# Kernel tuning notes

Hardware: AMD Instinct MI355X
Metric: run time of the kernel (lower is better)

## Reference

```python
import jax, jax.numpy as jnp
import numpy as np

DIM = 1024
HEADS = 16
DIM_HEAD = 64
INNER = HEADS * DIM_HEAD
SCALE = DIM_HEAD ** -0.5


def rotate_half(t):
    # '... (j d) -> ... j d' with j=2: split last dim in half
    x1, x2 = jnp.split(t, 2, axis=-1)
    return jnp.concatenate((-x2, x1), axis=-1)


def rotary_pos(n, d, dtype):
    inv_freq = 1.0 / (10000.0 ** (jnp.arange(0, d, 2, dtype=jnp.float32) / d))
    freqs = jnp.arange(n, dtype=jnp.float32)[:, None] * inv_freq[None, :]  # (n, d/2)
    return jnp.concatenate((freqs, freqs), axis=-1).astype(dtype)  # (n, d)


def apply_rope(pos, t):
    return t * jnp.cos(pos) + rotate_half(t) * jnp.sin(pos)


def setup_inputs() -> dict:
    key = jax.random.key(0)
    ks = jax.random.split(key, 5)
    x = jax.random.normal(ks[0], (2, 2048, DIM), dtype=jnp.float32)
    gamma = jnp.ones((DIM,), dtype=jnp.float32)
    beta = jnp.zeros((DIM,), dtype=jnp.float32)
    Wq = jax.random.normal(ks[1], (DIM, INNER), dtype=jnp.float32) * 0.02
    Wkv = jax.random.normal(ks[2], (DIM, 2 * INNER), dtype=jnp.float32) * 0.02
    Wo = jax.random.normal(ks[3], (INNER, DIM), dtype=jnp.float32) * 0.02
    return {"x": x, "gamma": gamma, "beta": beta, "Wq": Wq, "Wkv": Wkv, "Wo": Wo}


def reference(x, gamma, beta, Wq, Wkv, Wo):
    b, n, _ = x.shape
    # LayerNorm with learned gamma, fixed-zero beta buffer
    mu = jnp.mean(x, axis=-1, keepdims=True)
    var = jnp.var(x, axis=-1, keepdims=True)
    xn = (x - mu) / jnp.sqrt(var + 1e-5) * gamma + beta

    q = xn @ Wq                       # (b, n, inner)
    kv = xn @ Wkv
    k, v = jnp.split(kv, 2, axis=-1)

    def to_heads(t):
        return t.reshape(b, n, HEADS, DIM_HEAD).transpose(0, 2, 1, 3)  # b h n d

    q, k, v = map(to_heads, (q, k, v))

    pos = rotary_pos(n, DIM_HEAD, x.dtype)  # (n, d)
    q = apply_rope(pos, q)
    k = apply_rope(pos, k)

    q = q * SCALE
    sim = jnp.einsum('bhid,bhjd->bhij', q, k)

    neg = -jnp.finfo(sim.dtype).max
    causal_mask = jnp.triu(jnp.ones((n, n), dtype=bool), k=1)
    sim = jnp.where(causal_mask, neg, sim)

    attn = jax.nn.softmax(sim, axis=-1)
    out = jnp.einsum('bhij,bhjd->bhid', attn, v)
    out = out.transpose(0, 2, 1, 3).reshape(b, n, INNER)
    return out @ Wo
```

## Files before the change

### kernel.cpp

```cpp
#include <hip/hip_runtime.h>
#include <stdint.h>

typedef unsigned short u16;
typedef __attribute__((ext_vector_type(8))) short short8;
typedef __attribute__((ext_vector_type(4))) float floatx4;
typedef __attribute__((ext_vector_type(4))) unsigned short u16x4;
typedef __attribute__((ext_vector_type(2))) unsigned int uint2v;

__device__ __forceinline__ float bf2f(u16 v) {
  union { uint32_t u; float f; } x; x.u = ((uint32_t)v) << 16; return x.f;
}
__device__ __forceinline__ u16 f2bf(float f) {
  union { float f; uint32_t u; } x; x.f = f;
  uint32_t r = x.u + 0x7fffu + ((x.u >> 16) & 1u);
  return (u16)(r >> 16);
}
__device__ __forceinline__ uint32_t fu(float f) {
  union { float f; uint32_t u; } x; x.f = f; return x.u;
}

#define GL2LDS(g, l)                                                          \
  __builtin_amdgcn_global_load_lds(                                           \
      (const __attribute__((address_space(1))) void*)(g),                     \
      (__attribute__((address_space(3))) void*)(l), 16, 0, 0)

__global__ __launch_bounds__(256) void transpose_w3_k(const float* __restrict__ Wq,
                                                      const float* __restrict__ Wkv,
                                                      const float* __restrict__ Wo,
                                                      u16* __restrict__ wqkvT,
                                                      u16* __restrict__ woT) {
  __shared__ float tile[32][33];
  int z = blockIdx.z;
  const float* in = (z == 0) ? Wq : (z == 1) ? Wkv : Wo;
  u16* out = (z == 0) ? wqkvT : (z == 1) ? (wqkvT + 1024 * 1024) : woT;
  int C = (z == 1) ? 2048 : 1024;
  int c0 = blockIdx.x * 32, r0 = blockIdx.y * 32;
  if (c0 >= C) return;
  int tx = threadIdx.x, ty = threadIdx.y;
#pragma unroll
  for (int i = 0; i < 32; i += 8)
    tile[ty + i][tx] = in[(size_t)(r0 + ty + i) * C + c0 + tx];
  __syncthreads();
#pragma unroll
  for (int i = 0; i < 32; i += 8)
    out[(size_t)(c0 + ty + i) * 1024 + r0 + tx] = f2bf(tile[tx][ty + i]);
}

__global__ __launch_bounds__(256) void layernorm_k(const float* __restrict__ x,
                                                   const float* __restrict__ gamma,
                                                   const float* __restrict__ beta,
                                                   u16* __restrict__ xn) {
  int row = blockIdx.x;
  int t = threadIdx.x;
  const float* xr = x + (size_t)row * 1024;
  float4 xv = *(const float4*)(xr + t * 4);
  float v0 = xv.x, v1 = xv.y, v2 = xv.z, v3 = xv.w;
  float s = v0 + v1 + v2 + v3;
  float s2 = v0 * v0 + v1 * v1 + v2 * v2 + v3 * v3;
#pragma unroll
  for (int d = 1; d < 64; d <<= 1) {
    s += __shfl_xor(s, d, 64);
    s2 += __shfl_xor(s2, d, 64);
  }
  __shared__ float red[8];
  int lane = t & 63, wv = t >> 6;
  if (lane == 0) { red[wv] = s; red[4 + wv] = s2; }
  __syncthreads();
  s = red[0] + red[1] + red[2] + red[3];
  s2 = red[4] + red[5] + red[6] + red[7];
  float mu = s * (1.0f / 1024.0f);
  float var = s2 * (1.0f / 1024.0f) - mu * mu;
  float rstd = rsqrtf(var + 1e-5f);
  float4 gv = *(const float4*)(gamma + t * 4);
  float4 bv = *(const float4*)(beta + t * 4);
  u16x4 ov;
  ov.x = f2bf((v0 - mu) * rstd * gv.x + bv.x);
  ov.y = f2bf((v1 - mu) * rstd * gv.y + bv.y);
  ov.z = f2bf((v2 - mu) * rstd * gv.z + bv.z);
  ov.w = f2bf((v3 - mu) * rstd * gv.w + bv.w);
  *(u16x4*)(xn + (size_t)row * 1024 + t * 4) = ov;
}

__global__ __launch_bounds__(256) void gemm_bf16_k(const u16* __restrict__ A,
                                                   const u16* __restrict__ BT,
                                                   void* __restrict__ Cp,
                                                   int K, int lda, int ldc,
                                                   int f32out) {
  __shared__ __align__(16) u16 lA[128 * 32];
  __shared__ __align__(16) u16 lB[128 * 32];
  int tid = threadIdx.x;
  int bm = blockIdx.y * 128;
  int bn = blockIdx.x * 128;
  int w = tid >> 6, l = tid & 63;
  int wm = (w >> 1) * 64, wn = (w & 1) * 64;
  int lr = l & 15, lq = l >> 4;
  floatx4 acc[4][4] = {};
  int sr = w * 16 + (l >> 2);
  int sc = (l & 3) * 8;
  for (int k0 = 0; k0 < K; k0 += 32) {
    GL2LDS(A + (size_t)(bm + sr) * lda + k0 + sc, &lA[sr * 32 + sc]);
    GL2LDS(A + (size_t)(bm + sr + 64) * lda + k0 + sc, &lA[(sr + 64) * 32 + sc]);
    GL2LDS(BT + (size_t)(bn + sr) * K + k0 + sc, &lB[sr * 32 + sc]);
    GL2LDS(BT + (size_t)(bn + sr + 64) * K + k0 + sc, &lB[(sr + 64) * 32 + sc]);
    __syncthreads();
    short8 afr[4], bfr[4];
#pragma unroll
    for (int i = 0; i < 4; i++)
      afr[i] = *(const short8*)(&lA[(wm + i * 16 + lr) * 32 + lq * 8]);
#pragma unroll
    for (int i = 0; i < 4; i++)
      bfr[i] = *(const short8*)(&lB[(wn + i * 16 + lr) * 32 + lq * 8]);
#pragma unroll
    for (int mi = 0; mi < 4; mi++)
#pragma unroll
      for (int ni = 0; ni < 4; ni++)
        acc[mi][ni] = __builtin_amdgcn_mfma_f32_16x16x32_bf16(
            afr[mi], bfr[ni], acc[mi][ni], 0, 0, 0);
    __syncthreads();
  }
  if (f32out) {
    float* Cf = (float*)Cp;
#pragma unroll
    for (int mi = 0; mi < 4; mi++)
#pragma unroll
      for (int ni = 0; ni < 4; ni++)
#pragma unroll
        for (int r = 0; r < 4; r++) {
          int row = bm + wm + mi * 16 + lq * 4 + r;
          int col = bn + wn + ni * 16 + lr;
          Cf[(size_t)row * ldc + col] = acc[mi][ni][r];
        }
  } else {
    u16* Cb = (u16*)Cp;
#pragma unroll
    for (int mi = 0; mi < 4; mi++)
#pragma unroll
      for (int ni = 0; ni < 4; ni++)
#pragma unroll
        for (int r = 0; r < 4; r++) {
          int row = bm + wm + mi * 16 + lq * 4 + r;
          int col = bn + wn + ni * 16 + lr;
          Cb[(size_t)row * ldc + col] = f2bf(acc[mi][ni][r]);
        }
  }
}

__global__ __launch_bounds__(256) void gemm64_bf16_k(const u16* __restrict__ A,
                                                     const u16* __restrict__ BT,
                                                     float* __restrict__ C,
                                                     int K, int lda, int ldc) {
  __shared__ __align__(16) u16 lA[64 * 32];
  __shared__ __align__(16) u16 lB[128 * 32];
  int tid = threadIdx.x;
  int bm = blockIdx.y * 64;
  int bn = blockIdx.x * 128;
  int w = tid >> 6, l = tid & 63;
  int wm = (w >> 1) * 32, wn = (w & 1) * 64;
  int lr = l & 15, lq = l >> 4;
  floatx4 acc[2][4] = {};
  int sr = w * 16 + (l >> 2);
  int sc = (l & 3) * 8;
  for (int k0 = 0; k0 < K; k0 += 32) {
    GL2LDS(A + (size_t)(bm + sr) * lda + k0 + sc, &lA[sr * 32 + sc]);
    GL2LDS(BT + (size_t)(bn + sr) * K + k0 + sc, &lB[sr * 32 + sc]);
    GL2LDS(BT + (size_t)(bn + sr + 64) * K + k0 + sc, &lB[(sr + 64) * 32 + sc]);
    __syncthreads();
    short8 afr[2], bfr[4];
#pragma unroll
    for (int i = 0; i < 2; i++)
      afr[i] = *(const short8*)(&lA[(wm + i * 16 + lr) * 32 + lq * 8]);
#pragma unroll
    for (int i = 0; i < 4; i++)
      bfr[i] = *(const short8*)(&lB[(wn + i * 16 + lr) * 32 + lq * 8]);
#pragma unroll
    for (int mi = 0; mi < 2; mi++)
#pragma unroll
      for (int ni = 0; ni < 4; ni++)
        acc[mi][ni] = __builtin_amdgcn_mfma_f32_16x16x32_bf16(
            afr[mi], bfr[ni], acc[mi][ni], 0, 0, 0);
    __syncthreads();
  }
#pragma unroll
  for (int mi = 0; mi < 2; mi++)
#pragma unroll
    for (int ni = 0; ni < 4; ni++)
#pragma unroll
      for (int r = 0; r < 4; r++) {
        int row = bm + wm + mi * 16 + lq * 4 + r;
        int col = bn + wn + ni * 16 + lr;
        C[(size_t)row * ldc + col] = acc[mi][ni][r];
      }
}

__global__ __launch_bounds__(256) void rope_inplace_k(u16* __restrict__ qkv) {
  int idx = blockIdx.x * 256 + threadIdx.x;
  int ig = idx & 7;
  int h = (idx >> 3) & 15;
  int row = idx >> 7;
  int n = row & 2047;
  int i0 = ig * 4;
  const float QS = 0.125f * 1.44269504088896f;
  float c_[4], s_[4];
  float invf = exp2f(-(float)i0 * 0.4152410118609203f);
  const float rstep = 0.74989420933245582f;
#pragma unroll
  for (int e = 0; e < 4; e++) {
    float ang = (float)n * invf;
    c_[e] = cosf(ang);
    s_[e] = sinf(ang);
    invf *= rstep;
  }
  size_t base = (size_t)row * 3072 + h * 64 + i0;
  u16x4 qlo = *(u16x4*)(qkv + base);
  u16x4 qhi = *(u16x4*)(qkv + base + 32);
  u16x4 klo = *(u16x4*)(qkv + base + 1024);
  u16x4 khi = *(u16x4*)(qkv + base + 1056);
  u16x4 oqlo, oqhi, oklo, okhi;
#pragma unroll
  for (int e = 0; e < 4; e++) {
    float x1 = bf2f(((u16*)&qlo)[e]), x2 = bf2f(((u16*)&qhi)[e]);
    ((u16*)&oqlo)[e] = f2bf((x1 * c_[e] - x2 * s_[e]) * QS);
    ((u16*)&oqhi)[e] = f2bf((x2 * c_[e] + x1 * s_[e]) * QS);
    x1 = bf2f(((u16*)&klo)[e]); x2 = bf2f(((u16*)&khi)[e]);
    ((u16*)&oklo)[e] = f2bf(x1 * c_[e] - x2 * s_[e]);
    ((u16*)&okhi)[e] = f2bf(x2 * c_[e] + x1 * s_[e]);
  }
  *(u16x4*)(qkv + base) = oqlo;
  *(u16x4*)(qkv + base + 32) = oqhi;
  *(u16x4*)(qkv + base + 1024) = oklo;
  *(u16x4*)(qkv + base + 1056) = okhi;
}

__global__ __launch_bounds__(256) void transpose_v_k(const u16* __restrict__ qkv,
                                                     u16* __restrict__ vT) {
  __shared__ u16 tile[32][33];
  int bh = blockIdx.z;
  int b = bh >> 4, h = bh & 15;
  int n0 = blockIdx.x * 32, d0 = blockIdx.y * 32;
  int tx = threadIdx.x, ty = threadIdx.y;
#pragma unroll
  for (int i = 0; i < 32; i += 8)
    tile[ty + i][tx] =
        qkv[(size_t)(b * 2048 + n0 + ty + i) * 3072 + 2048 + h * 64 + d0 + tx];
  __syncthreads();
#pragma unroll
  for (int i = 0; i < 32; i += 8)
    vT[((size_t)bh * 64 + d0 + ty + i) * 2048 + n0 + tx] = tile[tx][ty + i];
}

#define LPT 72
__device__ __forceinline__ void attn_tile2(const u16* lK, const u16* lV, u16* lp,
                                           const short8* aq, floatx4* o,
                                           float& m_i, float& l_i, int lr, int lq,
                                           bool diag, int q0, int k0g,
                                           short8 ones) {
  floatx4 s[4];
#pragma unroll
  for (int ni = 0; ni < 4; ni++) {
    floatx4 a = {};
#pragma unroll
    for (int kc = 0; kc < 2; kc++) {
      int R = ni * 16 + lr;
      int c8 = (kc * 4 + lq) ^ (R & 7);
      short8 kf = *(const short8*)&lK[R * 64 + c8 * 8];
      a = __builtin_amdgcn_mfma_f32_16x16x32_bf16(kf, aq[kc], a, 0, 0, 0);
    }
    s[ni] = a;
  }
  if (diag) {
    int qg = q0 + lr;
#pragma unroll
    for (int ni = 0; ni < 4; ni++)
#pragma unroll
      for (int r = 0; r < 4; r++) {
        int kg = k0g + ni * 16 + lq * 4 + r;
        if (kg > qg) s[ni][r] = -1e30f;
      }
  }
  float mx = fmaxf(fmaxf(s[0][0], s[0][1]), fmaxf(s[0][2], s[0][3]));
#pragma unroll
  for (int ni = 1; ni < 4; ni++)
    mx = fmaxf(mx, fmaxf(fmaxf(s[ni][0], s[ni][1]), fmaxf(s[ni][2], s[ni][3])));
  mx = fmaxf(mx, __shfl_xor(mx, 16, 64));
  mx = fmaxf(mx, __shfl_xor(mx, 32, 64));
  float mnew = fmaxf(m_i, mx);
  float alpha = exp2f(m_i - mnew);
  m_i = mnew;
#pragma unroll
  for (int ni = 0; ni < 4; ni++) {
    float p0 = exp2f(s[ni][0] - mnew), p1 = exp2f(s[ni][1] - mnew);
    float p2 = exp2f(s[ni][2] - mnew), p3 = exp2f(s[ni][3] - mnew);
    uint2v dw;
    dw.x = __builtin_amdgcn_perm(fu(p1), fu(p0), 0x07060302u);
    dw.y = __builtin_amdgcn_perm(fu(p3), fu(p2), 0x07060302u);
    *(uint2v*)&lp[lr * LPT + ni * 16 + lq * 4] = dw;
  }
  short8 pb0 = *(const short8*)&lp[lr * LPT + lq * 8];
  short8 pb1 = *(const short8*)&lp[lr * LPT + 32 + lq * 8];
  floatx4 z = {};
  z = __builtin_amdgcn_mfma_f32_16x16x32_bf16(ones, pb0, z, 0, 0, 0);
  z = __builtin_amdgcn_mfma_f32_16x16x32_bf16(ones, pb1, z, 0, 0, 0);
  l_i = l_i * alpha + z[0];
#pragma unroll
  for (int di = 0; di < 4; di++)
#pragma unroll
    for (int r = 0; r < 4; r++) o[di][r] *= alpha;
#pragma unroll
  for (int di = 0; di < 4; di++) {
    int R = di * 16 + lr;
    int c80 = lq ^ (R & 7);
    int c81 = (4 + lq) ^ (R & 7);
    short8 v0 = *(const short8*)&lV[R * 64 + c80 * 8];
    o[di] = __builtin_amdgcn_mfma_f32_16x16x32_bf16(v0, pb0, o[di], 0, 0, 0);
    short8 v1 = *(const short8*)&lV[R * 64 + c81 * 8];
    o[di] = __builtin_amdgcn_mfma_f32_16x16x32_bf16(v1, pb1, o[di], 0, 0, 0);
  }
}

__global__ __launch_bounds__(256) void attn_k(const u16* __restrict__ qkv,
                                              const u16* __restrict__ vt,
                                              u16* __restrict__ out) {
  __shared__ __align__(16) u16 lK[2][64 * 64];
  __shared__ __align__(16) u16 lV[2][64 * 64];
  __shared__ __align__(16) u16 lP[4][16 * LPT];
  int bh = blockIdx.y;
  int b = bh >> 4, h = bh & 15;
  int p = blockIdx.x;
  int jB = 31 - p;
  int tid = threadIdx.x;
  int w = tid >> 6, l = tid & 63;
  int lr = l & 15, lq = l >> 4;
  int q0A = p * 64 + w * 16;
  int q0B = jB * 64 + w * 16;
  const u16* qb = qkv + (size_t)b * 2048 * 3072 + h * 64;
  const u16* kb = qkv + (size_t)b * 2048 * 3072 + 1024 + h * 64;
  const u16* vb = vt + (size_t)bh * 64 * 2048;
  short8 aqA[2], aqB[2];
  aqA[0] = *(const short8*)(qb + (size_t)(q0A + lr) * 3072 + lq * 8);
  aqA[1] = *(const short8*)(qb + (size_t)(q0A + lr) * 3072 + 32 + lq * 8);
  aqB[0] = *(const short8*)(qb + (size_t)(q0B + lr) * 3072 + lq * 8);
  aqB[1] = *(const short8*)(qb + (size_t)(q0B + lr) * 3072 + 32 + lq * 8);
  short8 ones;
#pragma unroll
  for (int i = 0; i < 8; i++) ones[i] = (short)0x3F80;
  floatx4 oA[4] = {}, oB[4] = {};
  float mA = -1e30f, lA_ = 0.0f, mB = -1e30f, lB_ = 0.0f;
  int srow8 = l >> 3;
  int sc8 = (l & 7) ^ srow8;
  u16* lp = &lP[w][0];
  auto stage = [&](int bufi, int kt) {
#pragma unroll
    for (int c = 0; c < 2; c++) {
      int m = w + c * 4;
      int row = m * 8 + srow8;
      GL2LDS(kb + (size_t)(kt * 64 + row) * 3072 + sc8 * 8, &lK[bufi][m * 512]);
      GL2LDS(vb + (size_t)row * 2048 + kt * 64 + sc8 * 8, &lV[bufi][m * 512]);
    }
  };
  stage(0, 0);
  for (int kt = 0; kt <= jB; ++kt) {
    int cur = kt & 1;
    __syncthreads();
    if (kt < jB) stage(cur ^ 1, kt + 1);
    attn_tile2(lK[cur], lV[cur], lp, aqB, oB, mB, lB_, lr, lq, kt == jB, q0B,
               kt * 64, ones);
    if (kt <= p)
      attn_tile2(lK[cur], lV[cur], lp, aqA, oA, mA, lA_, lr, lq, kt == p, q0A,
                 kt * 64, ones);
  }
  float rlA = 1.0f / lA_, rlB = 1.0f / lB_;
#pragma unroll
  for (int di = 0; di < 4; di++) {
    uint2v dwA, dwB;
    u16 a0 = f2bf(oA[di][0] * rlA), a1 = f2bf(oA[di][1] * rlA);
    u16 a2 = f2bf(oA[di][2] * rlA), a3 = f2bf(oA[di][3] * rlA);
    dwA.x = (uint32_t)a0 | ((uint32_t)a1 << 16);
    dwA.y = (uint32_t)a2 | ((uint32_t)a3 << 16);
    u16 b0 = f2bf(oB[di][0] * rlB), b1 = f2bf(oB[di][1] * rlB);
    u16 b2 = f2bf(oB[di][2] * rlB), b3 = f2bf(oB[di][3] * rlB);
    dwB.x = (uint32_t)b0 | ((uint32_t)b1 << 16);
    dwB.y = (uint32_t)b2 | ((uint32_t)b3 << 16);
    int dcol = h * 64 + di * 16 + lq * 4;
    *(uint2v*)(out + ((size_t)(b * 2048 + q0A + lr)) * 3072 + dcol) = dwA;
    *(uint2v*)(out + ((size_t)(b * 2048 + q0B + lr)) * 3072 + dcol) = dwB;
  }
}

extern "C" void kernel_launch(void* const* d_in, const int* in_sizes, int n_in,
                              void* d_out, int out_size, void* d_ws, size_t ws_size,
                              hipStream_t stream) {
  const float* x = (const float*)d_in[0];
  const float* gamma = (const float*)d_in[1];
  const float* beta = (const float*)d_in[2];
  const float* Wq = (const float*)d_in[3];
  const float* Wkv = (const float*)d_in[4];
  const float* Wo = (const float*)d_in[5];
  float* out = (float*)d_out;
  char* ws = (char*)d_ws;

  u16* qkv = (u16*)(ws);
  u16* wqkvT = (u16*)(ws + 25165824);
  u16* woT = (u16*)(ws + 31457280);
  u16* xn = (u16*)(ws + 33554432);
  u16* vT = xn;
  u16* attn_out = qkv + 2048;

  dim3 tb32(32, 8);
  transpose_w3_k<<<dim3(64, 32, 3), tb32, 0, stream>>>(Wq, Wkv, Wo, wqkvT, woT);
  layernorm_k<<<4096, 256, 0, stream>>>(x, gamma, beta, xn);
  gemm_bf16_k<<<dim3(24, 32), 256, 0, stream>>>(xn, wqkvT, qkv, 1024, 1024, 3072, 0);
  rope_inplace_k<<<2048, 256, 0, stream>>>(qkv);
  transpose_v_k<<<dim3(64, 2, 32), tb32, 0, stream>>>(qkv, vT);
  attn_k<<<dim3(16, 32), 256, 0, stream>>>(qkv, vT, attn_out);
  gemm64_bf16_k<<<dim3(8, 64), 256, 0, stream>>>(attn_out, woT, out, 1024, 3072, 1024);
}
```

Measured before the change: 214.3 us.

## Fuse RoPE and V-transpose kernels; hoist K/V fragments to registers in attention

Merges the in-place RoPE kernel and the V transpose kernel into one launch, splitting work by block index, which removes one kernel launch. In the attention loop, K and V fragments are read from LDS once per tile into registers and shared by both query halves instead of being reloaded for each. Separate per-wave P buffers for the A and B halves remove the reuse hazard between the two tile calls. Holding the fragments in registers raises register pressure and may lower occupancy.

Measured after the change: 215.9 us. About the same (+0.8%).

```diff
diff --git a/kernel.cpp b/kernel.cpp
--- a/kernel.cpp
+++ b/kernel.cpp
@@ -192,64 +192,70 @@
       }
 }
 
-__global__ __launch_bounds__(256) void rope_inplace_k(u16* __restrict__ qkv) {
-  int idx = blockIdx.x * 256 + threadIdx.x;
-  int ig = idx & 7;
-  int h = (idx >> 3) & 15;
-  int row = idx >> 7;
-  int n = row & 2047;
-  int i0 = ig * 4;
-  const float QS = 0.125f * 1.44269504088896f;
-  float c_[4], s_[4];
-  float invf = exp2f(-(float)i0 * 0.4152410118609203f);
-  const float rstep = 0.74989420933245582f;
-#pragma unroll
-  for (int e = 0; e < 4; e++) {
-    float ang = (float)n * invf;
-    c_[e] = cosf(ang);
-    s_[e] = sinf(ang);
-    invf *= rstep;
-  }
-  size_t base = (size_t)row * 3072 + h * 64 + i0;
-  u16x4 qlo = *(u16x4*)(qkv + base);
-  u16x4 qhi = *(u16x4*)(qkv + base + 32);
-  u16x4 klo = *(u16x4*)(qkv + base + 1024);
-  u16x4 khi = *(u16x4*)(qkv + base + 1056);
-  u16x4 oqlo, oqhi, oklo, okhi;
-#pragma unroll
-  for (int e = 0; e < 4; e++) {
-    float x1 = bf2f(((u16*)&qlo)[e]), x2 = bf2f(((u16*)&qhi)[e]);
-    ((u16*)&oqlo)[e] = f2bf((x1 * c_[e] - x2 * s_[e]) * QS);
-    ((u16*)&oqhi)[e] = f2bf((x2 * c_[e] + x1 * s_[e]) * QS);
-    x1 = bf2f(((u16*)&klo)[e]); x2 = bf2f(((u16*)&khi)[e]);
-    ((u16*)&oklo)[e] = f2bf(x1 * c_[e] - x2 * s_[e]);
-    ((u16*)&okhi)[e] = f2bf(x2 * c_[e] + x1 * s_[e]);
-  }
-  *(u16x4*)(qkv + base) = oqlo;
-  *(u16x4*)(qkv + base + 32) = oqhi;
-  *(u16x4*)(qkv + base + 1024) = oklo;
-  *(u16x4*)(qkv + base + 1056) = okhi;
-}
-
-__global__ __launch_bounds__(256) void transpose_v_k(const u16* __restrict__ qkv,
-                                                     u16* __restrict__ vT) {
-  __shared__ u16 tile[32][33];
-  int bh = blockIdx.z;
-  int b = bh >> 4, h = bh & 15;
-  int n0 = blockIdx.x * 32, d0 = blockIdx.y * 32;
-  int tx = threadIdx.x, ty = threadIdx.y;
-#pragma unroll
-  for (int i = 0; i < 32; i += 8)
-    tile[ty + i][tx] =
-        qkv[(size_t)(b * 2048 + n0 + ty + i) * 3072 + 2048 + h * 64 + d0 + tx];
-  __syncthreads();
-#pragma unroll
-  for (int i = 0; i < 32; i += 8)
-    vT[((size_t)bh * 64 + d0 + ty + i) * 2048 + n0 + tx] = tile[tx][ty + i];
+__global__ __launch_bounds__(256) void rope_vt_k(u16* __restrict__ qkv,
+                                                 u16* __restrict__ vT) {
+  int bid = blockIdx.x;
+  if (bid < 2048) {
+    int idx = bid * 256 + threadIdx.x;
+    int ig = idx & 7;
+    int h = (idx >> 3) & 15;
+    int row = idx >> 7;
+    int n = row & 2047;
+    int i0 = ig * 4;
+    const float QS = 0.125f * 1.44269504088896f;
+    float c_[4], s_[4];
+    float invf = exp2f(-(float)i0 * 0.4152410118609203f);
+    const float rstep = 0.74989420933245582f;
+#pragma unroll
+    for (int e = 0; e < 4; e++) {
+      float ang = (float)n * invf;
+      c_[e] = cosf(ang);
+      s_[e] = sinf(ang);
+      invf *= rstep;
+    }
+    size_t base = (size_t)row * 3072 + h * 64 + i0;
+    u16x4 qlo = *(u16x4*)(qkv + base);
+    u16x4 qhi = *(u16x4*)(qkv + base + 32);
+    u16x4 klo = *(u16x4*)(qkv + base + 1024);
+    u16x4 khi = *(u16x4*)(qkv + base + 1056);
+    u16x4 oqlo, oqhi, oklo, okhi;
+#pragma unroll
+    for (int e = 0; e < 4; e++) {
+      float x1 = bf2f(((u16*)&qlo)[e]), x2 = bf2f(((u16*)&qhi)[e]);
+      ((u16*)&oqlo)[e] = f2bf((x1 * c_[e] - x2 * s_[e]) * QS);
+      ((u16*)&oqhi)[e] = f2bf((x2 * c_[e] + x1 * s_[e]) * QS);
+      x1 = bf2f(((u16*)&klo)[e]); x2 = bf2f(((u16*)&khi)[e]);
+      ((u16*)&oklo)[e] = f2bf(x1 * c_[e] - x2 * s_[e]);
+      ((u16*)&okhi)[e] = f2bf(x2 * c_[e] + x1 * s_[e]);
+    }
+    *(u16x4*)(qkv + base) = oqlo;
+    *(u16x4*)(qkv + base + 32) = oqhi;
+    *(u16x4*)(qkv + base + 1024) = oklo;
+    *(u16x4*)(qkv + base + 1056) = okhi;
+  } else {
+    __shared__ u16 tile[32][33];
+    int vb = bid - 2048;
+    int bh = vb >> 7;
+    int rest = vb & 127;
+    int d0 = (rest >> 6) * 32;
+    int n0 = (rest & 63) * 32;
+    int b = bh >> 4, h = bh & 15;
+    int tid = threadIdx.x;
+    int tx = tid & 31, ty = tid >> 5;
+#pragma unroll
+    for (int i = 0; i < 32; i += 8)
+      tile[ty + i][tx] =
+          qkv[(size_t)(b * 2048 + n0 + ty + i) * 3072 + 2048 + h * 64 + d0 + tx];
+    __syncthreads();
+#pragma unroll
+    for (int i = 0; i < 32; i += 8)
+      vT[((size_t)bh * 64 + d0 + ty + i) * 2048 + n0 + tx] = tile[tx][ty + i];
+  }
 }
 
 #define LPT 72
-__device__ __forceinline__ void attn_tile2(const u16* lK, const u16* lV, u16* lp,
+__device__ __forceinline__ void attn_tile2(const short8 kf[4][2],
+                                           const short8 vf[4][2], u16* lp,
                                            const short8* aq, floatx4* o,
                                            float& m_i, float& l_i, int lr, int lq,
                                            bool diag, int q0, int k0g,
@@ -259,12 +265,8 @@
   for (int ni = 0; ni < 4; ni++) {
     floatx4 a = {};
 #pragma unroll
-    for (int kc = 0; kc < 2; kc++) {
-      int R = ni * 16 + lr;
-      int c8 = (kc * 4 + lq) ^ (R & 7);
-      short8 kf = *(const short8*)&lK[R * 64 + c8 * 8];
-      a = __builtin_amdgcn_mfma_f32_16x16x32_bf16(kf, aq[kc], a, 0, 0, 0);
-    }
+    for (int kc = 0; kc < 2; kc++)
+      a = __builtin_amdgcn_mfma_f32_16x16x32_bf16(kf[ni][kc], aq[kc], a, 0, 0, 0);
     s[ni] = a;
   }
   if (diag) {
@@ -307,13 +309,8 @@
     for (int r = 0; r < 4; r++) o[di][r] *= alpha;
 #pragma unroll
   for (int di = 0; di < 4; di++) {
-    int R = di * 16 + lr;
-    int c80 = lq ^ (R & 7);
-    int c81 = (4 + lq) ^ (R & 7);
-    short8 v0 = *(const short8*)&lV[R * 64 + c80 * 8];
-    o[di] = __builtin_amdgcn_mfma_f32_16x16x32_bf16(v0, pb0, o[di], 0, 0, 0);
-    short8 v1 = *(const short8*)&lV[R * 64 + c81 * 8];
-    o[di] = __builtin_amdgcn_mfma_f32_16x16x32_bf16(v1, pb1, o[di], 0, 0, 0);
+    o[di] = __builtin_amdgcn_mfma_f32_16x16x32_bf16(vf[di][0], pb0, o[di], 0, 0, 0);
+    o[di] = __builtin_amdgcn_mfma_f32_16x16x32_bf16(vf[di][1], pb1, o[di], 0, 0, 0);
   }
 }
 
@@ -322,7 +319,8 @@
                                               u16* __restrict__ out) {
   __shared__ __align__(16) u16 lK[2][64 * 64];
   __shared__ __align__(16) u16 lV[2][64 * 64];
-  __shared__ __align__(16) u16 lP[4][16 * LPT];
+  __shared__ __align__(16) u16 lPA[4][16 * LPT];
+  __shared__ __align__(16) u16 lPB[4][16 * LPT];
   int bh = blockIdx.y;
   int b = bh >> 4, h = bh & 15;
   int p = blockIdx.x;
@@ -347,7 +345,6 @@
   float mA = -1e30f, lA_ = 0.0f, mB = -1e30f, lB_ = 0.0f;
   int srow8 = l >> 3;
   int sc8 = (l & 7) ^ srow8;
-  u16* lp = &lP[w][0];
   auto stage = [&](int bufi, int kt) {
 #pragma unroll
     for (int c = 0; c < 2; c++) {
@@ -362,10 +359,21 @@
     int cur = kt & 1;
     __syncthreads();
     if (kt < jB) stage(cur ^ 1, kt + 1);
-    attn_tile2(lK[cur], lV[cur], lp, aqB, oB, mB, lB_, lr, lq, kt == jB, q0B,
+    short8 kf[4][2], vf[4][2];
+#pragma unroll
+    for (int ni = 0; ni < 4; ni++) {
+      int R = ni * 16 + lr;
+      int c80 = (lq ^ (R & 7)) * 8;
+      int c81 = ((4 + lq) ^ (R & 7)) * 8;
+      kf[ni][0] = *(const short8*)&lK[cur][R * 64 + c80];
+      kf[ni][1] = *(const short8*)&lK[cur][R * 64 + c81];
+      vf[ni][0] = *(const short8*)&lV[cur][R * 64 + c80];
+      vf[ni][1] = *(const short8*)&lV[cur][R * 64 + c81];
+    }
+    attn_tile2(kf, vf, &lPB[w][0], aqB, oB, mB, lB_, lr, lq, kt == jB, q0B,
                kt * 64, ones);
     if (kt <= p)
-      attn_tile2(lK[cur], lV[cur], lp, aqA, oA, mA, lA_, lr, lq, kt == p, q0A,
+      attn_tile2(kf, vf, &lPA[w][0], aqA, oA, mA, lA_, lr, lq, kt == p, q0A,
                  kt * 64, ones);
   }
   float rlA = 1.0f / lA_, rlB = 1.0f / lB_;
@@ -409,8 +417,7 @@
   transpose_w3_k<<<dim3(64, 32, 3), tb32, 0, stream>>>(Wq, Wkv, Wo, wqkvT, woT);
   layernorm_k<<<4096, 256, 0, stream>>>(x, gamma, beta, xn);
   gemm_bf16_k<<<dim3(24, 32), 256, 0, stream>>>(xn, wqkvT, qkv, 1024, 1024, 3072, 0);
-  rope_inplace_k<<<2048, 256, 0, stream>>>(qkv);
-  transpose_v_k<<<dim3(64, 2, 32), tb32, 0, stream>>>(qkv, vT);
+  rope_vt_k<<<6144, 256, 0, stream>>>(qkv, vT);
   attn_k<<<dim3(16, 32), 256, 0, stream>>>(qkv, vT, attn_out);
   gemm64_bf16_k<<<dim3(8, 64), 256, 0, stream>>>(attn_out, woT, out, 1024, 3072, 1024);
 }
```

## Fuse RoPE into QKV GEMM epilogue and merge layernorm with weight transpose

Applied to the files above, without the earlier changes.

RoPE rotation and the query scaling move into the QKV GEMM epilogue. Each wave's 64-column tile covers one head, so the x1/x2 halves are already in registers (acc[ni] and acc[ni+2]), which removes the separate in-place RoPE pass over qkv. Layernorm and the three weight transposes are merged into one launch by splitting on block index, and the V transpose uses a flattened 1D grid. The result is two fewer kernel launches and one less read-modify-write of Q/K. In exchange the epilogue uses fast __sincosf in fp32 on the unrounded accumulator, which may shift numerics slightly.

New measurement: 216.2 us. Within noise of the previous version (+0.9%).

```diff
diff --git a/kernel.cpp b/kernel.cpp
--- a/kernel.cpp
+++ b/kernel.cpp
@@ -24,68 +24,72 @@
       (const __attribute__((address_space(1))) void*)(g),                     \
       (__attribute__((address_space(3))) void*)(l), 16, 0, 0)
 
-__global__ __launch_bounds__(256) void transpose_w3_k(const float* __restrict__ Wq,
-                                                      const float* __restrict__ Wkv,
-                                                      const float* __restrict__ Wo,
-                                                      u16* __restrict__ wqkvT,
-                                                      u16* __restrict__ woT) {
-  __shared__ float tile[32][33];
-  int z = blockIdx.z;
-  const float* in = (z == 0) ? Wq : (z == 1) ? Wkv : Wo;
-  u16* out = (z == 0) ? wqkvT : (z == 1) ? (wqkvT + 1024 * 1024) : woT;
-  int C = (z == 1) ? 2048 : 1024;
-  int c0 = blockIdx.x * 32, r0 = blockIdx.y * 32;
-  if (c0 >= C) return;
-  int tx = threadIdx.x, ty = threadIdx.y;
-#pragma unroll
-  for (int i = 0; i < 32; i += 8)
-    tile[ty + i][tx] = in[(size_t)(r0 + ty + i) * C + c0 + tx];
-  __syncthreads();
-#pragma unroll
-  for (int i = 0; i < 32; i += 8)
-    out[(size_t)(c0 + ty + i) * 1024 + r0 + tx] = f2bf(tile[tx][ty + i]);
-}
-
-__global__ __launch_bounds__(256) void layernorm_k(const float* __restrict__ x,
-                                                   const float* __restrict__ gamma,
-                                                   const float* __restrict__ beta,
-                                                   u16* __restrict__ xn) {
-  int row = blockIdx.x;
+__global__ __launch_bounds__(256) void prep_k(const float* __restrict__ x,
+                                              const float* __restrict__ gamma,
+                                              const float* __restrict__ beta,
+                                              const float* __restrict__ Wq,
+                                              const float* __restrict__ Wkv,
+                                              const float* __restrict__ Wo,
+                                              u16* __restrict__ xn,
+                                              u16* __restrict__ wqkvT,
+                                              u16* __restrict__ woT) {
+  int bid = blockIdx.x;
   int t = threadIdx.x;
-  const float* xr = x + (size_t)row * 1024;
-  float4 xv = *(const float4*)(xr + t * 4);
-  float v0 = xv.x, v1 = xv.y, v2 = xv.z, v3 = xv.w;
-  float s = v0 + v1 + v2 + v3;
-  float s2 = v0 * v0 + v1 * v1 + v2 * v2 + v3 * v3;
-#pragma unroll
-  for (int d = 1; d < 64; d <<= 1) {
-    s += __shfl_xor(s, d, 64);
-    s2 += __shfl_xor(s2, d, 64);
-  }
-  __shared__ float red[8];
-  int lane = t & 63, wv = t >> 6;
-  if (lane == 0) { red[wv] = s; red[4 + wv] = s2; }
-  __syncthreads();
-  s = red[0] + red[1] + red[2] + red[3];
-  s2 = red[4] + red[5] + red[6] + red[7];
-  float mu = s * (1.0f / 1024.0f);
-  float var = s2 * (1.0f / 1024.0f) - mu * mu;
-  float rstd = rsqrtf(var + 1e-5f);
-  float4 gv = *(const float4*)(gamma + t * 4);
-  float4 bv = *(const float4*)(beta + t * 4);
-  u16x4 ov;
-  ov.x = f2bf((v0 - mu) * rstd * gv.x + bv.x);
-  ov.y = f2bf((v1 - mu) * rstd * gv.y + bv.y);
-  ov.z = f2bf((v2 - mu) * rstd * gv.z + bv.z);
-  ov.w = f2bf((v3 - mu) * rstd * gv.w + bv.w);
-  *(u16x4*)(xn + (size_t)row * 1024 + t * 4) = ov;
-}
-
-__global__ __launch_bounds__(256) void gemm_bf16_k(const u16* __restrict__ A,
-                                                   const u16* __restrict__ BT,
-                                                   void* __restrict__ Cp,
-                                                   int K, int lda, int ldc,
-                                                   int f32out) {
+  if (bid < 4096) {
+    int row = bid;
+    const float* xr = x + (size_t)row * 1024;
+    float4 xv = *(const float4*)(xr + t * 4);
+    float v0 = xv.x, v1 = xv.y, v2 = xv.z, v3 = xv.w;
+    float s = v0 + v1 + v2 + v3;
+    float s2 = v0 * v0 + v1 * v1 + v2 * v2 + v3 * v3;
+#pragma unroll
+    for (int d = 1; d < 64; d <<= 1) {
+      s += __shfl_xor(s, d, 64);
+      s2 += __shfl_xor(s2, d, 64);
+    }
+    __shared__ float red[8];
+    int lane = t & 63, wv = t >> 6;
+    if (lane == 0) { red[wv] = s; red[4 + wv] = s2; }
+    __syncthreads();
+    s = red[0] + red[1] + red[2] + red[3];
+    s2 = red[4] + red[5] + red[6] + red[7];
+    float mu = s * (1.0f / 1024.0f);
+    float var = s2 * (1.0f / 1024.0f) - mu * mu;
+    float rstd = rsqrtf(var + 1e-5f);
+    float4 gv = *(const float4*)(gamma + t * 4);
+    float4 bv = *(const float4*)(beta + t * 4);
+    u16x4 ov;
+    ov.x = f2bf((v0 - mu) * rstd * gv.x + bv.x);
+    ov.y = f2bf((v1 - mu) * rstd * gv.y + bv.y);
+    ov.z = f2bf((v2 - mu) * rstd * gv.z + bv.z);
+    ov.w = f2bf((v3 - mu) * rstd * gv.w + bv.w);
+    *(u16x4*)(xn + (size_t)row * 1024 + t * 4) = ov;
+  } else {
+    __shared__ float tile[32][33];
+    int wb = bid - 4096;
+    const float* in;
+    u16* outp;
+    int C;
+    if (wb < 1024) { in = Wq; outp = wqkvT; C = 1024; }
+    else if (wb < 3072) { wb -= 1024; in = Wkv; outp = wqkvT + 1024 * 1024; C = 2048; }
+    else { wb -= 3072; in = Wo; outp = woT; C = 1024; }
+    int nbx = C >> 5;
+    int c0 = (wb % nbx) * 32, r0 = (wb / nbx) * 32;
+    int tx = t & 31, ty = t >> 5;
+#pragma unroll
+    for (int i = 0; i < 32; i += 8)
+      tile[ty + i][tx] = in[(size_t)(r0 + ty + i) * C + c0 + tx];
+    __syncthreads();
+#pragma unroll
+    for (int i = 0; i < 32; i += 8)
+      outp[(size_t)(c0 + ty + i) * 1024 + r0 + tx] = f2bf(tile[tx][ty + i]);
+  }
+}
+
+__global__ __launch_bounds__(256) void gemm_qkv_k(const u16* __restrict__ A,
+                                                  const u16* __restrict__ BT,
+                                                  u16* __restrict__ C) {
+  const int K = 1024, lda = 1024, ldc = 3072;
   __shared__ __align__(16) u16 lA[128 * 32];
   __shared__ __align__(16) u16 lB[128 * 32];
   int tid = threadIdx.x;
@@ -118,8 +122,8 @@
             afr[mi], bfr[ni], acc[mi][ni], 0, 0, 0);
     __syncthreads();
   }
-  if (f32out) {
-    float* Cf = (float*)Cp;
+  int sec = bn >> 10;
+  if (sec == 2) {
 #pragma unroll
     for (int mi = 0; mi < 4; mi++)
 #pragma unroll
@@ -128,20 +132,29 @@
         for (int r = 0; r < 4; r++) {
           int row = bm + wm + mi * 16 + lq * 4 + r;
           int col = bn + wn + ni * 16 + lr;
-          Cf[(size_t)row * ldc + col] = acc[mi][ni][r];
+          C[(size_t)row * ldc + col] = f2bf(acc[mi][ni][r]);
         }
   } else {
-    u16* Cb = (u16*)Cp;
-#pragma unroll
-    for (int mi = 0; mi < 4; mi++)
-#pragma unroll
-      for (int ni = 0; ni < 4; ni++)
+    float QS = (sec == 0) ? 0.125f * 1.44269504088896f : 1.0f;
+#pragma unroll
+    for (int ni = 0; ni < 2; ni++) {
+      int i = ni * 16 + lr;
+      float invf = exp2f(-(float)i * 0.4152410118609203f);
+#pragma unroll
+      for (int mi = 0; mi < 4; mi++)
 #pragma unroll
         for (int r = 0; r < 4; r++) {
           int row = bm + wm + mi * 16 + lq * 4 + r;
+          int n = row & 2047;
+          float ang = (float)n * invf;
+          float s_, c_;
+          __sincosf(ang, &s_, &c_);
+          float x1 = acc[mi][ni][r], x2 = acc[mi][ni + 2][r];
           int col = bn + wn + ni * 16 + lr;
-          Cb[(size_t)row * ldc + col] = f2bf(acc[mi][ni][r]);
+          C[(size_t)row * ldc + col] = f2bf((x1 * c_ - x2 * s_) * QS);
+          C[(size_t)row * ldc + col + 32] = f2bf((x2 * c_ + x1 * s_) * QS);
         }
+    }
   }
 }
 
@@ -192,52 +205,17 @@
       }
 }
 
-__global__ __launch_bounds__(256) void rope_inplace_k(u16* __restrict__ qkv) {
-  int idx = blockIdx.x * 256 + threadIdx.x;
-  int ig = idx & 7;
-  int h = (idx >> 3) & 15;
-  int row = idx >> 7;
-  int n = row & 2047;
-  int i0 = ig * 4;
-  const float QS = 0.125f * 1.44269504088896f;
-  float c_[4], s_[4];
-  float invf = exp2f(-(float)i0 * 0.4152410118609203f);
-  const float rstep = 0.74989420933245582f;
-#pragma unroll
-  for (int e = 0; e < 4; e++) {
-    float ang = (float)n * invf;
-    c_[e] = cosf(ang);
-    s_[e] = sinf(ang);
-    invf *= rstep;
-  }
-  size_t base = (size_t)row * 3072 + h * 64 + i0;
-  u16x4 qlo = *(u16x4*)(qkv + base);
-  u16x4 qhi = *(u16x4*)(qkv + base + 32);
-  u16x4 klo = *(u16x4*)(qkv + base + 1024);
-  u16x4 khi = *(u16x4*)(qkv + base + 1056);
-  u16x4 oqlo, oqhi, oklo, okhi;
-#pragma unroll
-  for (int e = 0; e < 4; e++) {
-    float x1 = bf2f(((u16*)&qlo)[e]), x2 = bf2f(((u16*)&qhi)[e]);
-    ((u16*)&oqlo)[e] = f2bf((x1 * c_[e] - x2 * s_[e]) * QS);
-    ((u16*)&oqhi)[e] = f2bf((x2 * c_[e] + x1 * s_[e]) * QS);
-    x1 = bf2f(((u16*)&klo)[e]); x2 = bf2f(((u16*)&khi)[e]);
-    ((u16*)&oklo)[e] = f2bf(x1 * c_[e] - x2 * s_[e]);
-    ((u16*)&okhi)[e] = f2bf(x2 * c_[e] + x1 * s_[e]);
-  }
-  *(u16x4*)(qkv + base) = oqlo;
-  *(u16x4*)(qkv + base + 32) = oqhi;
-  *(u16x4*)(qkv + base + 1024) = oklo;
-  *(u16x4*)(qkv + base + 1056) = okhi;
-}
-
-__global__ __launch_bounds__(256) void transpose_v_k(const u16* __restrict__ qkv,
-                                                     u16* __restrict__ vT) {
+__global__ __launch_bounds__(256) void vt_k(const u16* __restrict__ qkv,
+                                            u16* __restrict__ vT) {
   __shared__ u16 tile[32][33];
-  int bh = blockIdx.z;
+  int vb = blockIdx.x;
+  int bh = vb >> 7;
+  int rest = vb & 127;
+  int d0 = (rest >> 6) * 32;
+  int n0 = (rest & 63) * 32;
   int b = bh >> 4, h = bh & 15;
-  int n0 = blockIdx.x * 32, d0 = blockIdx.y * 32;
-  int tx = threadIdx.x, ty = threadIdx.y;
+  int tid = threadIdx.x;
+  int tx = tid & 31, ty = tid >> 5;
 #pragma unroll
   for (int i = 0; i < 32; i += 8)
     tile[ty + i][tx] =
@@ -405,12 +383,9 @@
   u16* vT = xn;
   u16* attn_out = qkv + 2048;
 
-  dim3 tb32(32, 8);
-  transpose_w3_k<<<dim3(64, 32, 3), tb32, 0, stream>>>(Wq, Wkv, Wo, wqkvT, woT);
-  layernorm_k<<<4096, 256, 0, stream>>>(x, gamma, beta, xn);
-  gemm_bf16_k<<<dim3(24, 32), 256, 0, stream>>>(xn, wqkvT, qkv, 1024, 1024, 3072, 0);
-  rope_inplace_k<<<2048, 256, 0, stream>>>(qkv);
-  transpose_v_k<<<dim3(64, 2, 32), tb32, 0, stream>>>(qkv, vT);
+  prep_k<<<8192, 256, 0, stream>>>(x, gamma, beta, Wq, Wkv, Wo, xn, wqkvT, woT);
+  gemm_qkv_k<<<dim3(24, 32), 256, 0, stream>>>(xn, wqkvT, qkv);
+  vt_k<<<4096, 256, 0, stream>>>(qkv, vT);
   attn_k<<<dim3(16, 32), 256, 0, stream>>>(qkv, vT, attn_out);
   gemm64_bf16_k<<<dim3(8, 64), 256, 0, stream>>>(attn_out, woT, out, 1024, 3072, 1024);
 }
```
